# Kernel tuning notes

Hardware: AMD Instinct MI355X
Metric: run time of the kernel (lower is better)

## Reference

```python
import jax, jax.numpy as jnp
import numpy as np

N_NODES = 20000
N_RELS = 64
RP = 8
EMB = 64
N_CLASSES = 16
NT = 250000      # unique (subject, object) pairs
N_TRIPLES = 500000


def setup_inputs() -> dict:
    rng = np.random.default_rng(0)
    # sample candidate (s, o) pairs, dedupe (mirrors torch.unique(pairs, dim=0)),
    # keep exactly NT unique pairs
    cand = rng.integers(0, N_NODES, size=(NT + 60000, 2))
    pairs = np.unique(cand, axis=0)
    assert pairs.shape[0] >= NT
    pairs = pairs[:NT]
    # each triple maps to a unique-pair row and a relation column;
    # relation_matrix is the coalesced sparse_coo (nt, num_rels) densified
    row = rng.integers(0, NT, size=N_TRIPLES)
    rel = rng.integers(0, N_RELS, size=N_TRIPLES)
    relation_matrix = np.zeros((NT, N_RELS), dtype=np.float32)
    np.add.at(relation_matrix, (row, rel), 1.0)
    # hindices / vindices exactly as in __init__ (note the literal o*r / s*r):
    s, o = pairs[:, 0].astype(np.int64), pairs[:, 1].astype(np.int64)
    rm = np.arange(RP, dtype=np.int64)[:, None]
    hrow = np.tile(s, RP)                      # (RP*NT,) row in [0, N)
    hcol = (o[None, :] * rm).reshape(-1)       # (RP*NT,) col in [0, N*RP)
    vrow = (s[None, :] * rm).reshape(-1)       # (RP*NT,) row in [0, N*RP)
    vcol = np.tile(o, RP)                      # (RP*NT,) col in [0, N)

    key = jax.random.key(0)
    ks = jax.random.split(key, 6)

    def xavier(k, shape, fan_in, fan_out):
        gain = np.float32(np.sqrt(2.0))  # calculate_gain('relu')
        bound = gain * np.float32(np.sqrt(6.0 / (fan_in + fan_out)))
        return jax.random.uniform(k, shape, jnp.float32, -bound, bound)

    lb = np.float32(1.0 / np.sqrt(N_RELS))  # nn.Linear default init bound
    return {
        "relation_matrix": jnp.asarray(relation_matrix),
        "hrow": jnp.asarray(hrow), "hcol": jnp.asarray(hcol),
        "vrow": jnp.asarray(vrow), "vcol": jnp.asarray(vcol),
        "W_l1": jax.random.uniform(ks[0], (N_RELS, RP), jnp.float32, -lb, lb),
        "b_l1": jax.random.uniform(ks[1], (RP,), jnp.float32, -lb, lb),
        "W_l2": jax.random.uniform(ks[2], (N_RELS, RP), jnp.float32, -lb, lb),
        "b_l2": jax.random.uniform(ks[3], (RP,), jnp.float32, -lb, lb),
        "weights1": xavier(ks[4], (RP, N_NODES, EMB), N_NODES * EMB, RP * EMB),
        "weights2": xavier(ks[5], (RP, EMB, N_CLASSES), EMB * N_CLASSES, RP * N_CLASSES),
        "bias1": jnp.zeros((EMB,), jnp.float32),
        "bias2": jnp.zeros((N_CLASSES,), jnp.float32),
    }


def reference(relation_matrix, hrow, hcol, vrow, vcol,
              W_l1, b_l1, W_l2, b_l2, weights1, weights2, bias1, bias2):
    n, rp, e = N_NODES, RP, EMB
    nrp = n * rp
    # ---- hop 1: latent coefficients (to_latent1, ldepth=0 => single Linear)
    l1 = relation_matrix @ W_l1 + b_l1              # (NT, RP)
    l1 = l1.T.reshape(-1)                           # (RP*NT,) r-major, matches h/v index order
    # sum_sparse(hindices, l1, (n, n*rp), row=False): per-edge column-sum normalization
    colsum = jax.ops.segment_sum(l1, hcol, num_segments=nrp)
    l1 = l1 / colsum[hcol]
    # spmm over hindices: out[hrow] += l1 * weights1.view(n*rp, e)[hcol]
    Wflat = weights1.reshape(nrp, e)                # (N*RP, EMB)
    h = jax.ops.segment_sum(l1[:, None] * Wflat[hcol], hrow, num_segments=n)
    h = jax.nn.relu(h + bias1)                      # (N, EMB)
    # ---- hop 2
    l2 = jax.nn.softmax(relation_matrix @ W_l2 + b_l2, axis=1)  # (NT, RP)
    l2 = jax.nn.relu(l2.T.reshape(-1))              # (RP*NT,)
    # sum_sparse(vindices, l2, (n*rp, n), row=True): per-edge row-sum normalization
    rowsum = jax.ops.segment_sum(l2, vrow, num_segments=nrp)
    l2 = l2 / jnp.maximum(rowsum[vrow], 1e-6)
    # spmm over vindices: out[vrow] += l2 * h[vcol]
    h2 = jax.ops.segment_sum(l2[:, None] * h[vcol], vrow, num_segments=nrp)
    h2 = h2.reshape(rp, n, e)                       # (RP, N, EMB)
    logits = jnp.einsum('rhc,rnh->nc', weights2, h2) + bias2  # (N, C)
    return logits
```

## Files before the change

### kernel.cpp

```cpp
#include <hip/hip_runtime.h>
#include <hip/hip_fp16.h>

#define NT      250000
#define NN      20000
#define RP      8
#define EMB     64
#define NCLS    16
#define NRELS   64
#define COLB    547
#define REDB    64
#define KMAX    140000

__global__ __launch_bounds__(256) void k_gemv(
    const float* __restrict__ rm,
    const float* __restrict__ W1, const float* __restrict__ b1,
    const float* __restrict__ W2, const float* __restrict__ b2,
    float* __restrict__ l1, float* __restrict__ l2)
{
    __shared__ float tile[256 * 20];
    int t = threadIdx.x;
    int base = blockIdx.x * 256;
    float a1[8], a2[8];
#pragma unroll
    for (int r = 0; r < 8; ++r) { a1[r] = b1[r]; a2[r] = b2[r]; }

#pragma unroll 1
    for (int kc = 0; kc < 4; ++kc) {
        __syncthreads();
#pragma unroll
        for (int q = 0; q < 4; ++q) {
            int i = q * 256 + t;
            int pl = i >> 2, j4 = i & 3;
            int p = base + pl;
            float4 v = make_float4(0.f, 0.f, 0.f, 0.f);
            if (p < NT) v = reinterpret_cast<const float4*>(rm)[(size_t)p * 16 + kc * 4 + j4];
            *reinterpret_cast<float4*>(&tile[pl * 20 + j4 * 4]) = v;
        }
        __syncthreads();
        float xr[16];
#pragma unroll
        for (int j4 = 0; j4 < 4; ++j4) {
            float4 v = *reinterpret_cast<const float4*>(&tile[t * 20 + j4 * 4]);
            xr[j4 * 4 + 0] = v.x; xr[j4 * 4 + 1] = v.y;
            xr[j4 * 4 + 2] = v.z; xr[j4 * 4 + 3] = v.w;
        }
#pragma unroll
        for (int kk = 0; kk < 16; ++kk) {
            float x = xr[kk];
            int k = kc * 16 + kk;
#pragma unroll
            for (int r = 0; r < 8; ++r) {
                a1[r] = fmaf(x, W1[k * 8 + r], a1[r]);
                a2[r] = fmaf(x, W2[k * 8 + r], a2[r]);
            }
        }
    }
    int p = base + t;
    if (p >= NT) return;
    float mx = a2[0];
#pragma unroll
    for (int r = 1; r < 8; ++r) mx = fmaxf(mx, a2[r]);
    float sm = 0.f;
#pragma unroll
    for (int r = 0; r < 8; ++r) { a2[r] = __expf(a2[r] - mx); sm += a2[r]; }
    float inv = 1.0f / sm;
#pragma unroll
    for (int r = 0; r < 8; ++r) a2[r] *= inv;
    float4* o1 = reinterpret_cast<float4*>(l1 + (size_t)p * 8);
    float4* o2 = reinterpret_cast<float4*>(l2 + (size_t)p * 8);
    o1[0] = make_float4(a1[0], a1[1], a1[2], a1[3]);
    o1[1] = make_float4(a1[4], a1[5], a1[6], a1[7]);
    o2[0] = make_float4(a2[0], a2[1], a2[2], a2[3]);
    o2[1] = make_float4(a2[4], a2[5], a2[6], a2[7]);
}

__global__ __launch_bounds__(256) void k_rowptr(
    const int* __restrict__ hrow, int* __restrict__ rowptr)
{
    int i = blockIdx.x * blockDim.x + threadIdx.x;
    if (i > NN) return;
    int lo = 0, hi = NT;
    while (lo < hi) { int mid = (lo + hi) >> 1; if (hrow[mid] < i) lo = mid + 1; else hi = mid; }
    rowptr[i] = lo;
}

__global__ __launch_bounds__(256) void k_hist(
    const int* __restrict__ vcol, int* __restrict__ cnt)
{
    int p = blockIdx.x * blockDim.x + threadIdx.x;
    if (p < NT) atomicAdd(&cnt[vcol[p]], 1);
}

__global__ __launch_bounds__(1024) void k_scan(
    const int* __restrict__ cnt, int* __restrict__ cstart, int* __restrict__ cnt2)
{
    __shared__ int part[1024];
    int t = threadIdx.x;
    int base = t * 20;
    int local[20];
    int s = 0;
#pragma unroll
    for (int i = 0; i < 20; ++i) {
        int idx = base + i;
        int c = (idx < NN) ? cnt[idx] : 0;
        local[i] = s;
        s += c;
    }
    part[t] = s;
    __syncthreads();
    for (int off = 1; off < 1024; off <<= 1) {
        int v = (t >= off) ? part[t - off] : 0;
        __syncthreads();
        part[t] += v;
        __syncthreads();
    }
    int ebase = t ? part[t - 1] : 0;
#pragma unroll
    for (int i = 0; i < 20; ++i) {
        int idx = base + i;
        if (idx < NN) { cstart[idx] = ebase + local[i]; cnt2[idx] = ebase + local[i]; }
    }
    if (t == 1023) cstart[NN] = part[1023];
}

__global__ __launch_bounds__(256) void k_pos(
    const int* __restrict__ vcol, int* __restrict__ cnt2, int* __restrict__ cscidx)
{
    int p = blockIdx.x * blockDim.x + threadIdx.x;
    if (p >= NT) return;
    int o = vcol[p];
    int slot = atomicAdd(&cnt2[o], 1);
    cscidx[slot] = p;
}

__global__ __launch_bounds__(256) void k_colsum(
    const float* __restrict__ l1, const int* __restrict__ cstart,
    const int* __restrict__ cscidx, float* __restrict__ colsum)
{
    int bid = blockIdx.x;
    if (bid < COLB) {
        int tid = bid * 256 + threadIdx.x;
        if (tid < NN * 7) {
            int o = tid / 7;
            int r = tid - o * 7 + 1;
            int qb = cstart[o], qe = cstart[o + 1];
            float s = 0.f;
            for (int q = qb; q < qe; ++q)
                s += l1[(size_t)cscidx[q] * 8 + r];
            atomicAdd(&colsum[o * r], s);
        }
    } else {
        int b2 = bid - COLB;
        float s = 0.f;
        for (int i = b2 * 256 + threadIdx.x; i < NT; i += REDB * 256) s += l1[(size_t)i * 8];
        __shared__ float red[256];
        red[threadIdx.x] = s;
        __syncthreads();
        for (int off = 128; off > 0; off >>= 1) {
            if (threadIdx.x < off) red[threadIdx.x] += red[threadIdx.x + off];
            __syncthreads();
        }
        if (threadIdx.x == 0) atomicAdd(&colsum[0], red[0]);
    }
}

__global__ __launch_bounds__(256) void k_inv(float* __restrict__ cs)
{
    int i = blockIdx.x * blockDim.x + threadIdx.x;
    if (i < RP * NN) cs[i] = 1.0f / cs[i];
}

__global__ __launch_bounds__(256) void k_contrib(
    const float* __restrict__ l1, const float* __restrict__ ics,
    const int* __restrict__ cstart, const int* __restrict__ cscidx,
    const float* __restrict__ w1, __half* __restrict__ contrib)
{
    int o = (int)((blockIdx.x * blockDim.x + threadIdx.x) >> 6);
    int lane = threadIdx.x & 63;
    if (o >= NN) return;
    int qb = cstart[o], qe = cstart[o + 1];
    if (qb == qe) return;
    float y[8];
    y[0] = w1[lane] * ics[0];
#pragma unroll
    for (int r = 1; r < 8; ++r) {
        int seg = o * r;
        y[r] = w1[(size_t)seg * EMB + lane] * ics[seg];
    }
    for (int q = qb; q < qe; ++q) {
        int p = cscidx[q];
        const float4* lp4 = reinterpret_cast<const float4*>(l1 + (size_t)p * 8);
        float4 A = lp4[0], B = lp4[1];
        float v = A.x * y[0];
        v = fmaf(A.y, y[1], v); v = fmaf(A.z, y[2], v); v = fmaf(A.w, y[3], v);
        v = fmaf(B.x, y[4], v); v = fmaf(B.y, y[5], v);
        v = fmaf(B.z, y[6], v); v = fmaf(B.w, y[7], v);
        contrib[(size_t)p * EMB + lane] = __float2half(v);
    }
}

__global__ __launch_bounds__(256) void k_h(
    const __half* __restrict__ contrib, const float* __restrict__ l2,
    const int* __restrict__ rowptr, const float* __restrict__ bias1,
    __half* __restrict__ h, float* __restrict__ rowsum, float* __restrict__ rs0part)
{
    int s = (int)((blockIdx.x * blockDim.x + threadIdx.x) >> 6);
    int lane = threadIdx.x & 63;
    if (s >= NN) return;
    int pb = rowptr[s], pe = rowptr[s + 1];
    float acc = 0.f;
    for (int p = pb; p < pe; ++p)
        acc += __half2float(contrib[(size_t)p * EMB + lane]);
    h[(size_t)s * EMB + lane] = __float2half(fmaxf(acc + bias1[lane], 0.f));

    float psum = 0.f;
    for (int p0 = pb + (lane >> 3); p0 < pe; p0 += 8)
        psum += l2[(size_t)p0 * 8 + (lane & 7)];
    psum += __shfl_xor(psum, 8, 64);
    psum += __shfl_xor(psum, 16, 64);
    psum += __shfl_xor(psum, 32, 64);
    if (s == 0) {
        float tt = psum;
        tt += __shfl_xor(tt, 1, 64);
        tt += __shfl_xor(tt, 2, 64);
        tt += __shfl_xor(tt, 4, 64);
        if (lane == 0) rs0part[0] = tt;
    } else {
        if (lane == 0) rs0part[s] = psum;
        else if (lane < 8) atomicAdd(&rowsum[s * lane], psum);
    }
}

__global__ __launch_bounds__(256) void k_redrs(
    const float* __restrict__ rs0part, float* __restrict__ rowsum)
{
    __shared__ float red[256];
    float sv = 0.f;
    for (int i = threadIdx.x; i < NN; i += 256) sv += rs0part[i];
    red[threadIdx.x] = sv;
    __syncthreads();
    for (int off = 128; off > 0; off >>= 1) {
        if (threadIdx.x < off) red[threadIdx.x] += red[threadIdx.x + off];
        __syncthreads();
    }
    if (threadIdx.x == 0) rowsum[0] = 1.0f / fmaxf(red[0], 1e-6f);
}

__global__ __launch_bounds__(256) void k_inv2(float* __restrict__ rs)
{
    int i = blockIdx.x * blockDim.x + threadIdx.x;
    if (i >= 1 && i < KMAX) rs[i] = 1.0f / fmaxf(rs[i], 1e-6f);
}

__global__ __launch_bounds__(256) void k_outinit(
    float* __restrict__ out, const float* __restrict__ b2)
{
    int i = blockIdx.x * blockDim.x + threadIdx.x;
    if (i < NN * NCLS) out[i] = b2[i & (NCLS - 1)];
}

__global__ __launch_bounds__(256) void k_l2out(
    const float* __restrict__ l2, const int* __restrict__ rowptr,
    const int* __restrict__ vcol, const __half* __restrict__ h,
    const float* __restrict__ irs, const float* __restrict__ w2,
    float* __restrict__ out, float* __restrict__ Abuf0)
{
    int s = (int)((blockIdx.x * blockDim.x + threadIdx.x) >> 6);
    int lane = threadIdx.x & 63;
    if (s >= NN) return;
    int pb = rowptr[s], pe = rowptr[s + 1];
    float acc[8];
#pragma unroll
    for (int r = 0; r < 8; ++r) acc[r] = 0.f;
    int p = pb;
    for (; p + 1 < pe; p += 2) {
        int o0 = vcol[p], o1 = vcol[p + 1];
        float hv0 = __half2float(h[(size_t)o0 * EMB + lane]);
        float hv1 = __half2float(h[(size_t)o1 * EMB + lane]);
        const float4* q4 = reinterpret_cast<const float4*>(l2 + (size_t)p * 8);
        float4 A = q4[0], B = q4[1], C = q4[2], D = q4[3];
        acc[0] = fmaf(A.x, hv0, fmaf(C.x, hv1, acc[0]));
        acc[1] = fmaf(A.y, hv0, fmaf(C.y, hv1, acc[1]));
        acc[2] = fmaf(A.z, hv0, fmaf(C.z, hv1, acc[2]));
        acc[3] = fmaf(A.w, hv0, fmaf(C.w, hv1, acc[3]));
        acc[4] = fmaf(B.x, hv0, fmaf(D.x, hv1, acc[4]));
        acc[5] = fmaf(B.y, hv0, fmaf(D.y, hv1, acc[5]));
        acc[6] = fmaf(B.z, hv0, fmaf(D.z, hv1, acc[6]));
        acc[7] = fmaf(B.w, hv0, fmaf(D.w, hv1, acc[7]));
    }
    if (p < pe) {
        int o0 = vcol[p];
        float hv0 = __half2float(h[(size_t)o0 * EMB + lane]);
        const float4* q4 = reinterpret_cast<const float4*>(l2 + (size_t)p * 8);
        float4 A = q4[0], B = q4[1];
        acc[0] = fmaf(A.x, hv0, acc[0]); acc[1] = fmaf(A.y, hv0, acc[1]);
        acc[2] = fmaf(A.z, hv0, acc[2]); acc[3] = fmaf(A.w, hv0, acc[3]);
        acc[4] = fmaf(B.x, hv0, acc[4]); acc[5] = fmaf(B.y, hv0, acc[5]);
        acc[6] = fmaf(B.z, hv0, acc[6]); acc[7] = fmaf(B.w, hv0, acc[7]);
    }
    if (s == 0) {
        float a = acc[0] + acc[1] + acc[2] + acc[3] +
                  acc[4] + acc[5] + acc[6] + acc[7];
        Abuf0[lane] = a;
        return;
    }
    Abuf0[(size_t)s * EMB + lane] = acc[0];
    if (pb == pe) return;
    int hq = lane >> 4, c = lane & 15;
#pragma unroll
    for (int rr = 1; rr < 8; ++rr) {
        int k = s * rr;
        int rp = k / NN;
        int n  = k - rp * NN;
        float sc = irs[k];
        float v = 0.f;
#pragma unroll
        for (int hh = 0; hh < 16; ++hh) {
            float av = __shfl(acc[rr], hq * 16 + hh, 64);
            v = fmaf(av, w2[((rp * EMB) + (hq * 16 + hh)) * NCLS + c], v);
        }
        v += __shfl_xor(v, 16, 64);
        v += __shfl_xor(v, 32, 64);
        if (lane < 16) atomicAdd(&out[(size_t)n * NCLS + lane], v * sc);
    }
}

__global__ __launch_bounds__(256) void k_redA(
    const float* __restrict__ Abuf0, float* __restrict__ h0row)
{
    __shared__ float red[256];
    int lane = threadIdx.x & 63, w = threadIdx.x >> 6;
    float sum = 0.f;
    for (int ss = blockIdx.x + 64 * w; ss < NN; ss += 256)
        sum += Abuf0[(size_t)ss * EMB + lane];
    red[threadIdx.x] = sum;
    __syncthreads();
    if (threadIdx.x < 64) {
        float v = red[threadIdx.x] + red[threadIdx.x + 64] +
                  red[threadIdx.x + 128] + red[threadIdx.x + 192];
        atomicAdd(&h0row[threadIdx.x], v);
    }
}

__global__ __launch_bounds__(64) void k_out0(
    const float* __restrict__ h0row, const float* __restrict__ irs,
    const float* __restrict__ w2, float* __restrict__ out)
{
    int hq = threadIdx.x >> 4, c = threadIdx.x & 15;
    float v = 0.f;
#pragma unroll
    for (int hh = 0; hh < 16; ++hh) {
        int hd = hq * 16 + hh;
        v = fmaf(h0row[hd], w2[hd * NCLS + c], v);
    }
    v += __shfl_xor(v, 16, 64);
    v += __shfl_xor(v, 32, 64);
    if (threadIdx.x < 16) atomicAdd(&out[c], v * irs[0]);
}

extern "C" void kernel_launch(void* const* d_in, const int* in_sizes, int n_in,
                              void* d_out, int out_size, void* d_ws, size_t ws_size,
                              hipStream_t stream)
{
    const float* rm    = (const float*)d_in[0];
    const int*   hrow  = (const int*)d_in[1];
    const int*   vcol  = (const int*)d_in[4];
    const float* W1    = (const float*)d_in[5];
    const float* b1    = (const float*)d_in[6];
    const float* W2    = (const float*)d_in[7];
    const float* b2    = (const float*)d_in[8];
    const float* w1    = (const float*)d_in[9];
    const float* w2    = (const float*)d_in[10];
    const float* bias1 = (const float*)d_in[11];
    const float* bias2 = (const float*)d_in[12];
    float* out = (float*)d_out;

    float* ws = (float*)d_ws;
    float*  l1      = ws;
    float*  l2      = ws + 2000000;
    int*    rowptr  = (int*)(ws + 4000000);
    float*  h0row   = ws + 4030000;
    float*  colsum  = ws + 4100000;
    float*  rowsum  = ws + 4260000;
    __half* h       = (__half*)(ws + 4400000);
    int*    cnt     = (int*)(ws + 5040000);
    int*    cstart  = cnt + 20000;
    int*    cnt2    = cstart + 20001;
    int*    cscidx  = cnt2 + 20000;
    __half* contrib = (__half*)(ws + 5600000);
    float*  Abuf0   = ws;
    float*  rs0part = ws + 1280000;

    hipMemsetAsync(colsum, 0, (size_t)160000 * sizeof(float), stream);
    hipMemsetAsync(rowsum, 0, (size_t)KMAX * sizeof(float), stream);
    hipMemsetAsync(h0row, 0, (size_t)64 * sizeof(float), stream);
    hipMemsetAsync(cnt, 0, (size_t)20000 * sizeof(int), stream);

    k_rowptr <<<(NN + 256) / 256, 256, 0, stream>>>(hrow, rowptr);
    k_hist   <<<(NT + 255) / 256, 256, 0, stream>>>(vcol, cnt);
    k_scan   <<<1, 1024, 0, stream>>>(cnt, cstart, cnt2);
    k_pos    <<<(NT + 255) / 256, 256, 0, stream>>>(vcol, cnt2, cscidx);
    k_gemv   <<<(NT + 255) / 256, 256, 0, stream>>>(rm, W1, b1, W2, b2, l1, l2);
    k_colsum <<<COLB + REDB, 256, 0, stream>>>(l1, cstart, cscidx, colsum);
    k_inv    <<<(RP * NN + 255) / 256, 256, 0, stream>>>(colsum);
    k_contrib<<<(NN * 64) / 256, 256, 0, stream>>>(l1, colsum, cstart, cscidx, w1, contrib);
    k_h      <<<(NN * 64) / 256, 256, 0, stream>>>(contrib, l2, rowptr, bias1, h, rowsum, rs0part);
    k_redrs  <<<1, 256, 0, stream>>>(rs0part, rowsum);
    k_inv2   <<<(KMAX + 255) / 256, 256, 0, stream>>>(rowsum);
    k_outinit<<<(NN * NCLS + 255) / 256, 256, 0, stream>>>(out, bias2);
    k_l2out  <<<(NN * 64) / 256, 256, 0, stream>>>(l2, rowptr, vcol, h, rowsum, w2, out, Abuf0);
    k_redA   <<<64, 256, 0, stream>>>(Abuf0, h0row);
    k_out0   <<<1, 64, 0, stream>>>(h0row, rowsum, w2, out);
}
```

Before: 261.8 us.

## Scatter l1 into CSC order and rewrite colsum as wave-per-column reduction

k_gemv now writes l1 rows directly in column-sorted (CSC) order using a position array recorded by k_pos. This lets colsum and contrib read l1 contiguously instead of gathering through cscidx. colsum becomes one wavefront per column with shuffle reductions, plus a separate reduction kernel for column 0. Smaller changes merge the inv2 and outinit kernels, unroll the k_l2out loop by 4, and hoist the row-scale loads. The cost is an extra index array, a scattered write in gemv, and one more tiny kernel launch.

```diff
diff --git a/kernel.cpp b/kernel.cpp
--- a/kernel.cpp
+++ b/kernel.cpp
@@ -7,15 +7,14 @@
 #define EMB     64
 #define NCLS    16
 #define NRELS   64
-#define COLB    547
-#define REDB    64
 #define KMAX    140000
 
 __global__ __launch_bounds__(256) void k_gemv(
     const float* __restrict__ rm,
     const float* __restrict__ W1, const float* __restrict__ b1,
     const float* __restrict__ W2, const float* __restrict__ b2,
-    float* __restrict__ l1, float* __restrict__ l2)
+    const int* __restrict__ cscpos,
+    float* __restrict__ l1csc, float* __restrict__ l2)
 {
     __shared__ float tile[256 * 20];
     int t = threadIdx.x;
@@ -66,7 +65,8 @@
     float inv = 1.0f / sm;
 #pragma unroll
     for (int r = 0; r < 8; ++r) a2[r] *= inv;
-    float4* o1 = reinterpret_cast<float4*>(l1 + (size_t)p * 8);
+    int q = cscpos[p];
+    float4* o1 = reinterpret_cast<float4*>(l1csc + (size_t)q * 8);
     float4* o2 = reinterpret_cast<float4*>(l2 + (size_t)p * 8);
     o1[0] = make_float4(a1[0], a1[1], a1[2], a1[3]);
     o1[1] = make_float4(a1[4], a1[5], a1[6], a1[7]);
@@ -124,44 +124,60 @@
 }
 
 __global__ __launch_bounds__(256) void k_pos(
-    const int* __restrict__ vcol, int* __restrict__ cnt2, int* __restrict__ cscidx)
+    const int* __restrict__ vcol, int* __restrict__ cnt2,
+    int* __restrict__ cscidx, int* __restrict__ cscpos)
 {
     int p = blockIdx.x * blockDim.x + threadIdx.x;
     if (p >= NT) return;
     int o = vcol[p];
     int slot = atomicAdd(&cnt2[o], 1);
     cscidx[slot] = p;
+    cscpos[p] = slot;
 }
 
 __global__ __launch_bounds__(256) void k_colsum(
-    const float* __restrict__ l1, const int* __restrict__ cstart,
-    const int* __restrict__ cscidx, float* __restrict__ colsum)
-{
-    int bid = blockIdx.x;
-    if (bid < COLB) {
-        int tid = bid * 256 + threadIdx.x;
-        if (tid < NN * 7) {
-            int o = tid / 7;
-            int r = tid - o * 7 + 1;
-            int qb = cstart[o], qe = cstart[o + 1];
-            float s = 0.f;
-            for (int q = qb; q < qe; ++q)
-                s += l1[(size_t)cscidx[q] * 8 + r];
-            atomicAdd(&colsum[o * r], s);
-        }
+    const float* __restrict__ l1csc, const int* __restrict__ cstart,
+    float* __restrict__ colsum, float* __restrict__ cs0part)
+{
+    int o = (int)((blockIdx.x * blockDim.x + threadIdx.x) >> 6);
+    int lane = threadIdx.x & 63;
+    if (o >= NN) return;
+    int qb = cstart[o], qe = cstart[o + 1];
+    if (qb == qe) { if (lane == 0) cs0part[o] = 0.f; return; }
+    int j = lane >> 3, r = lane & 7;
+    float sum = 0.f;
+    for (int q0 = qb; q0 < qe; q0 += 8) {
+        int q = q0 + j;
+        if (q < qe) sum += l1csc[(size_t)q * 8 + r];
+    }
+    sum += __shfl_xor(sum, 8, 64);
+    sum += __shfl_xor(sum, 16, 64);
+    sum += __shfl_xor(sum, 32, 64);
+    if (o == 0) {
+        float tt = sum;
+        tt += __shfl_xor(tt, 1, 64);
+        tt += __shfl_xor(tt, 2, 64);
+        tt += __shfl_xor(tt, 4, 64);
+        if (lane == 0) cs0part[0] = tt;
     } else {
-        int b2 = bid - COLB;
-        float s = 0.f;
-        for (int i = b2 * 256 + threadIdx.x; i < NT; i += REDB * 256) s += l1[(size_t)i * 8];
-        __shared__ float red[256];
-        red[threadIdx.x] = s;
-        __syncthreads();
-        for (int off = 128; off > 0; off >>= 1) {
-            if (threadIdx.x < off) red[threadIdx.x] += red[threadIdx.x + off];
-            __syncthreads();
-        }
-        if (threadIdx.x == 0) atomicAdd(&colsum[0], red[0]);
-    }
+        if (lane == 0) cs0part[o] = sum;
+        else if (lane < 8) atomicAdd(&colsum[o * lane], sum);
+    }
+}
+
+__global__ __launch_bounds__(256) void k_redcs(
+    const float* __restrict__ cs0part, float* __restrict__ colsum)
+{
+    __shared__ float red[256];
+    float sv = 0.f;
+    for (int i = threadIdx.x; i < NN; i += 256) sv += cs0part[i];
+    red[threadIdx.x] = sv;
+    __syncthreads();
+    for (int off = 128; off > 0; off >>= 1) {
+        if (threadIdx.x < off) red[threadIdx.x] += red[threadIdx.x + off];
+        __syncthreads();
+    }
+    if (threadIdx.x == 0) colsum[0] = red[0];
 }
 
 __global__ __launch_bounds__(256) void k_inv(float* __restrict__ cs)
@@ -171,7 +187,7 @@
 }
 
 __global__ __launch_bounds__(256) void k_contrib(
-    const float* __restrict__ l1, const float* __restrict__ ics,
+    const float* __restrict__ l1csc, const float* __restrict__ ics,
     const int* __restrict__ cstart, const int* __restrict__ cscidx,
     const float* __restrict__ w1, __half* __restrict__ contrib)
 {
@@ -188,13 +204,13 @@
         y[r] = w1[(size_t)seg * EMB + lane] * ics[seg];
     }
     for (int q = qb; q < qe; ++q) {
-        int p = cscidx[q];
-        const float4* lp4 = reinterpret_cast<const float4*>(l1 + (size_t)p * 8);
+        const float4* lp4 = reinterpret_cast<const float4*>(l1csc + (size_t)q * 8);
         float4 A = lp4[0], B = lp4[1];
         float v = A.x * y[0];
         v = fmaf(A.y, y[1], v); v = fmaf(A.z, y[2], v); v = fmaf(A.w, y[3], v);
         v = fmaf(B.x, y[4], v); v = fmaf(B.y, y[5], v);
         v = fmaf(B.z, y[6], v); v = fmaf(B.w, y[7], v);
+        int p = cscidx[q];
         contrib[(size_t)p * EMB + lane] = __float2half(v);
     }
 }
@@ -246,16 +262,11 @@
     if (threadIdx.x == 0) rowsum[0] = 1.0f / fmaxf(red[0], 1e-6f);
 }
 
-__global__ __launch_bounds__(256) void k_inv2(float* __restrict__ rs)
+__global__ __launch_bounds__(256) void k_misc(
+    float* __restrict__ rs, float* __restrict__ out, const float* __restrict__ b2)
 {
     int i = blockIdx.x * blockDim.x + threadIdx.x;
     if (i >= 1 && i < KMAX) rs[i] = 1.0f / fmaxf(rs[i], 1e-6f);
-}
-
-__global__ __launch_bounds__(256) void k_outinit(
-    float* __restrict__ out, const float* __restrict__ b2)
-{
-    int i = blockIdx.x * blockDim.x + threadIdx.x;
     if (i < NN * NCLS) out[i] = b2[i & (NCLS - 1)];
 }
 
@@ -269,26 +280,32 @@
     int lane = threadIdx.x & 63;
     if (s >= NN) return;
     int pb = rowptr[s], pe = rowptr[s + 1];
+    float sc[8];
+#pragma unroll
+    for (int rr = 1; rr < 8; ++rr) sc[rr] = (s > 0) ? irs[s * rr] : 0.f;
     float acc[8];
 #pragma unroll
     for (int r = 0; r < 8; ++r) acc[r] = 0.f;
     int p = pb;
-    for (; p + 1 < pe; p += 2) {
-        int o0 = vcol[p], o1 = vcol[p + 1];
+    for (; p + 3 < pe; p += 4) {
+        int o0 = vcol[p], o1 = vcol[p + 1], o2 = vcol[p + 2], o3 = vcol[p + 3];
         float hv0 = __half2float(h[(size_t)o0 * EMB + lane]);
         float hv1 = __half2float(h[(size_t)o1 * EMB + lane]);
+        float hv2 = __half2float(h[(size_t)o2 * EMB + lane]);
+        float hv3 = __half2float(h[(size_t)o3 * EMB + lane]);
         const float4* q4 = reinterpret_cast<const float4*>(l2 + (size_t)p * 8);
         float4 A = q4[0], B = q4[1], C = q4[2], D = q4[3];
-        acc[0] = fmaf(A.x, hv0, fmaf(C.x, hv1, acc[0]));
-        acc[1] = fmaf(A.y, hv0, fmaf(C.y, hv1, acc[1]));
-        acc[2] = fmaf(A.z, hv0, fmaf(C.z, hv1, acc[2]));
-        acc[3] = fmaf(A.w, hv0, fmaf(C.w, hv1, acc[3]));
-        acc[4] = fmaf(B.x, hv0, fmaf(D.x, hv1, acc[4]));
-        acc[5] = fmaf(B.y, hv0, fmaf(D.y, hv1, acc[5]));
-        acc[6] = fmaf(B.z, hv0, fmaf(D.z, hv1, acc[6]));
-        acc[7] = fmaf(B.w, hv0, fmaf(D.w, hv1, acc[7]));
-    }
-    if (p < pe) {
+        float4 E = q4[4], F = q4[5], G = q4[6], H = q4[7];
+        acc[0] = fmaf(A.x, hv0, fmaf(C.x, hv1, fmaf(E.x, hv2, fmaf(G.x, hv3, acc[0]))));
+        acc[1] = fmaf(A.y, hv0, fmaf(C.y, hv1, fmaf(E.y, hv2, fmaf(G.y, hv3, acc[1]))));
+        acc[2] = fmaf(A.z, hv0, fmaf(C.z, hv1, fmaf(E.z, hv2, fmaf(G.z, hv3, acc[2]))));
+        acc[3] = fmaf(A.w, hv0, fmaf(C.w, hv1, fmaf(E.w, hv2, fmaf(G.w, hv3, acc[3]))));
+        acc[4] = fmaf(B.x, hv0, fmaf(D.x, hv1, fmaf(F.x, hv2, fmaf(H.x, hv3, acc[4]))));
+        acc[5] = fmaf(B.y, hv0, fmaf(D.y, hv1, fmaf(F.y, hv2, fmaf(H.y, hv3, acc[5]))));
+        acc[6] = fmaf(B.z, hv0, fmaf(D.z, hv1, fmaf(F.z, hv2, fmaf(H.z, hv3, acc[6]))));
+        acc[7] = fmaf(B.w, hv0, fmaf(D.w, hv1, fmaf(F.w, hv2, fmaf(H.w, hv3, acc[7]))));
+    }
+    for (; p < pe; ++p) {
         int o0 = vcol[p];
         float hv0 = __half2float(h[(size_t)o0 * EMB + lane]);
         const float4* q4 = reinterpret_cast<const float4*>(l2 + (size_t)p * 8);
@@ -312,7 +329,6 @@
         int k = s * rr;
         int rp = k / NN;
         int n  = k - rp * NN;
-        float sc = irs[k];
         float v = 0.f;
 #pragma unroll
         for (int hh = 0; hh < 16; ++hh) {
@@ -321,7 +337,7 @@
         }
         v += __shfl_xor(v, 16, 64);
         v += __shfl_xor(v, 32, 64);
-        if (lane < 16) atomicAdd(&out[(size_t)n * NCLS + lane], v * sc);
+        if (lane < 16) atomicAdd(&out[(size_t)n * NCLS + lane], v * sc[rr]);
     }
 }
 
@@ -376,10 +392,11 @@
     float* out = (float*)d_out;
 
     float* ws = (float*)d_ws;
-    float*  l1      = ws;
+    float*  l1csc   = ws;
     float*  l2      = ws + 2000000;
     int*    rowptr  = (int*)(ws + 4000000);
     float*  h0row   = ws + 4030000;
+    float*  cs0part = ws + 4032000;
     float*  colsum  = ws + 4100000;
     float*  rowsum  = ws + 4260000;
     __half* h       = (__half*)(ws + 4400000);
@@ -387,7 +404,8 @@
     int*    cstart  = cnt + 20000;
     int*    cnt2    = cstart + 20001;
     int*    cscidx  = cnt2 + 20000;
-    __half* contrib = (__half*)(ws + 5600000);
+    int*    cscpos  = (int*)(ws + 5360000);
+    __half* contrib = (__half*)(ws + 5700000);
     float*  Abuf0   = ws;
     float*  rs0part = ws + 1280000;
 
@@ -399,15 +417,15 @@
     k_rowptr <<<(NN + 256) / 256, 256, 0, stream>>>(hrow, rowptr);
     k_hist   <<<(NT + 255) / 256, 256, 0, stream>>>(vcol, cnt);
     k_scan   <<<1, 1024, 0, stream>>>(cnt, cstart, cnt2);
-    k_pos    <<<(NT + 255) / 256, 256, 0, stream>>>(vcol, cnt2, cscidx);
-    k_gemv   <<<(NT + 255) / 256, 256, 0, stream>>>(rm, W1, b1, W2, b2, l1, l2);
-    k_colsum <<<COLB + REDB, 256, 0, stream>>>(l1, cstart, cscidx, colsum);
+    k_pos    <<<(NT + 255) / 256, 256, 0, stream>>>(vcol, cnt2, cscidx, cscpos);
+    k_gemv   <<<(NT + 255) / 256, 256, 0, stream>>>(rm, W1, b1, W2, b2, cscpos, l1csc, l2);
+    k_colsum <<<(NN * 64) / 256, 256, 0, stream>>>(l1csc, cstart, colsum, cs0part);
+    k_redcs  <<<1, 256, 0, stream>>>(cs0part, colsum);
     k_inv    <<<(RP * NN + 255) / 256, 256, 0, stream>>>(colsum);
-    k_contrib<<<(NN * 64) / 256, 256, 0, stream>>>(l1, colsum, cstart, cscidx, w1, contrib);
+    k_contrib<<<(NN * 64) / 256, 256, 0, stream>>>(l1csc, colsum, cstart, cscidx, w1, contrib);
     k_h      <<<(NN * 64) / 256, 256, 0, stream>>>(contrib, l2, rowptr, bias1, h, rowsum, rs0part);
     k_redrs  <<<1, 256, 0, stream>>>(rs0part, rowsum);
-    k_inv2   <<<(KMAX + 255) / 256, 256, 0, stream>>>(rowsum);
-    k_outinit<<<(NN * NCLS + 255) / 256, 256, 0, stream>>>(out, bias2);
+    k_misc   <<<(NN * NCLS + 255) / 256, 256, 0, stream>>>(rowsum, out, bias2);
     k_l2out  <<<(NN * 64) / 256, 256, 0, stream>>>(l2, rowptr, vcol, h, rowsum, w2, out, Abuf0);
     k_redA   <<<64, 256, 0, stream>>>(Abuf0, h0row);
     k_out0   <<<1, 64, 0, stream>>>(h0row, rowsum, w2, out);
```

Measured after the change: 269.4 us. 2.9% more time.

## Split each hop-2 row across two wavefronts and merge the init kernels

Applied to the files above, without the earlier changes.

The hop-2 SpMM kernel now gives each source row to two wavefronts. Each wavefront takes half the edges with a 4-way unrolled loop, and the partial accumulators are combined through shared memory. The seven class-projection atomics are also split between the two wavefronts, and the scale factors are prefetched before the edge loop. The inverse-rowsum and output-init kernels are fused into one launch. This adds more parallelism and memory-level overlap on long rows and removes one launch, at the cost of a block barrier, shared-memory traffic and idle wavefronts on short rows.

```diff
diff --git a/kernel.cpp b/kernel.cpp
--- a/kernel.cpp
+++ b/kernel.cpp
@@ -246,16 +246,11 @@
     if (threadIdx.x == 0) rowsum[0] = 1.0f / fmaxf(red[0], 1e-6f);
 }
 
-__global__ __launch_bounds__(256) void k_inv2(float* __restrict__ rs)
+__global__ __launch_bounds__(256) void k_misc(
+    float* __restrict__ rs, float* __restrict__ out, const float* __restrict__ b2)
 {
     int i = blockIdx.x * blockDim.x + threadIdx.x;
     if (i >= 1 && i < KMAX) rs[i] = 1.0f / fmaxf(rs[i], 1e-6f);
-}
-
-__global__ __launch_bounds__(256) void k_outinit(
-    float* __restrict__ out, const float* __restrict__ b2)
-{
-    int i = blockIdx.x * blockDim.x + threadIdx.x;
     if (i < NN * NCLS) out[i] = b2[i & (NCLS - 1)];
 }
 
@@ -265,30 +260,41 @@
     const float* __restrict__ irs, const float* __restrict__ w2,
     float* __restrict__ out, float* __restrict__ Abuf0)
 {
-    int s = (int)((blockIdx.x * blockDim.x + threadIdx.x) >> 6);
+    __shared__ float lacc[4][8 * 64];
+    int w = threadIdx.x >> 6;
     int lane = threadIdx.x & 63;
-    if (s >= NN) return;
+    int g = w >> 1, sub = w & 1;
+    int s = blockIdx.x * 2 + g;
     int pb = rowptr[s], pe = rowptr[s + 1];
+    float sc[8];
+#pragma unroll
+    for (int rr = 1; rr < 8; ++rr) sc[rr] = (s > 0) ? irs[s * rr] : 0.f;
     float acc[8];
 #pragma unroll
     for (int r = 0; r < 8; ++r) acc[r] = 0.f;
-    int p = pb;
-    for (; p + 1 < pe; p += 2) {
-        int o0 = vcol[p], o1 = vcol[p + 1];
+    int half = (pe - pb + 1) >> 1;
+    int mb = pb + sub * half;
+    int me = sub ? pe : pb + half;
+    int p = mb;
+    for (; p + 3 < me; p += 4) {
+        int o0 = vcol[p], o1 = vcol[p + 1], o2 = vcol[p + 2], o3 = vcol[p + 3];
         float hv0 = __half2float(h[(size_t)o0 * EMB + lane]);
         float hv1 = __half2float(h[(size_t)o1 * EMB + lane]);
+        float hv2 = __half2float(h[(size_t)o2 * EMB + lane]);
+        float hv3 = __half2float(h[(size_t)o3 * EMB + lane]);
         const float4* q4 = reinterpret_cast<const float4*>(l2 + (size_t)p * 8);
         float4 A = q4[0], B = q4[1], C = q4[2], D = q4[3];
-        acc[0] = fmaf(A.x, hv0, fmaf(C.x, hv1, acc[0]));
-        acc[1] = fmaf(A.y, hv0, fmaf(C.y, hv1, acc[1]));
-        acc[2] = fmaf(A.z, hv0, fmaf(C.z, hv1, acc[2]));
-        acc[3] = fmaf(A.w, hv0, fmaf(C.w, hv1, acc[3]));
-        acc[4] = fmaf(B.x, hv0, fmaf(D.x, hv1, acc[4]));
-        acc[5] = fmaf(B.y, hv0, fmaf(D.y, hv1, acc[5]));
-        acc[6] = fmaf(B.z, hv0, fmaf(D.z, hv1, acc[6]));
-        acc[7] = fmaf(B.w, hv0, fmaf(D.w, hv1, acc[7]));
-    }
-    if (p < pe) {
+        float4 E = q4[4], F = q4[5], G = q4[6], H = q4[7];
+        acc[0] = fmaf(A.x, hv0, fmaf(C.x, hv1, fmaf(E.x, hv2, fmaf(G.x, hv3, acc[0]))));
+        acc[1] = fmaf(A.y, hv0, fmaf(C.y, hv1, fmaf(E.y, hv2, fmaf(G.y, hv3, acc[1]))));
+        acc[2] = fmaf(A.z, hv0, fmaf(C.z, hv1, fmaf(E.z, hv2, fmaf(G.z, hv3, acc[2]))));
+        acc[3] = fmaf(A.w, hv0, fmaf(C.w, hv1, fmaf(E.w, hv2, fmaf(G.w, hv3, acc[3]))));
+        acc[4] = fmaf(B.x, hv0, fmaf(D.x, hv1, fmaf(F.x, hv2, fmaf(H.x, hv3, acc[4]))));
+        acc[5] = fmaf(B.y, hv0, fmaf(D.y, hv1, fmaf(F.y, hv2, fmaf(H.y, hv3, acc[5]))));
+        acc[6] = fmaf(B.z, hv0, fmaf(D.z, hv1, fmaf(F.z, hv2, fmaf(H.z, hv3, acc[6]))));
+        acc[7] = fmaf(B.w, hv0, fmaf(D.w, hv1, fmaf(F.w, hv2, fmaf(H.w, hv3, acc[7]))));
+    }
+    for (; p < me; ++p) {
         int o0 = vcol[p];
         float hv0 = __half2float(h[(size_t)o0 * EMB + lane]);
         const float4* q4 = reinterpret_cast<const float4*>(l2 + (size_t)p * 8);
@@ -298,30 +304,38 @@
         acc[4] = fmaf(B.x, hv0, acc[4]); acc[5] = fmaf(B.y, hv0, acc[5]);
         acc[6] = fmaf(B.z, hv0, acc[6]); acc[7] = fmaf(B.w, hv0, acc[7]);
     }
+#pragma unroll
+    for (int r = 0; r < 8; ++r) lacc[w][r * 64 + lane] = acc[r];
+    __syncthreads();
+    float ca[8];
+#pragma unroll
+    for (int r = 0; r < 8; ++r)
+        ca[r] = lacc[2 * g][r * 64 + lane] + lacc[2 * g + 1][r * 64 + lane];
     if (s == 0) {
-        float a = acc[0] + acc[1] + acc[2] + acc[3] +
-                  acc[4] + acc[5] + acc[6] + acc[7];
-        Abuf0[lane] = a;
+        if (sub == 0) {
+            float a = ca[0] + ca[1] + ca[2] + ca[3] + ca[4] + ca[5] + ca[6] + ca[7];
+            Abuf0[lane] = a;
+        }
         return;
     }
-    Abuf0[(size_t)s * EMB + lane] = acc[0];
+    if (sub == 0) Abuf0[(size_t)s * EMB + lane] = ca[0];
     if (pb == pe) return;
     int hq = lane >> 4, c = lane & 15;
-#pragma unroll
-    for (int rr = 1; rr < 8; ++rr) {
+    int rlo = sub ? 4 : 1, rhi = sub ? 8 : 4;
+    for (int rr = rlo; rr < rhi; ++rr) {
         int k = s * rr;
         int rp = k / NN;
         int n  = k - rp * NN;
-        float sc = irs[k];
+        float a = ca[rr];
         float v = 0.f;
 #pragma unroll
         for (int hh = 0; hh < 16; ++hh) {
-            float av = __shfl(acc[rr], hq * 16 + hh, 64);
+            float av = __shfl(a, hq * 16 + hh, 64);
             v = fmaf(av, w2[((rp * EMB) + (hq * 16 + hh)) * NCLS + c], v);
         }
         v += __shfl_xor(v, 16, 64);
         v += __shfl_xor(v, 32, 64);
-        if (lane < 16) atomicAdd(&out[(size_t)n * NCLS + lane], v * sc);
+        if (lane < 16) atomicAdd(&out[(size_t)n * NCLS + lane], v * sc[rr]);
     }
 }
 
@@ -343,7 +357,7 @@
 }
 
 __global__ __launch_bounds__(64) void k_out0(
-    const float* __restrict__ h0row, const float* __restrict__ irs,
+    const float* __restrict__ h0row, const float* __restrict__ irs0,
     const float* __restrict__ w2, float* __restrict__ out)
 {
     int hq = threadIdx.x >> 4, c = threadIdx.x & 15;
@@ -355,7 +369,7 @@
     }
     v += __shfl_xor(v, 16, 64);
     v += __shfl_xor(v, 32, 64);
-    if (threadIdx.x < 16) atomicAdd(&out[c], v * irs[0]);
+    if (threadIdx.x < 16) atomicAdd(&out[c], v * irs0[0]);
 }
 
 extern "C" void kernel_launch(void* const* d_in, const int* in_sizes, int n_in,
@@ -406,9 +420,8 @@
     k_contrib<<<(NN * 64) / 256, 256, 0, stream>>>(l1, colsum, cstart, cscidx, w1, contrib);
     k_h      <<<(NN * 64) / 256, 256, 0, stream>>>(contrib, l2, rowptr, bias1, h, rowsum, rs0part);
     k_redrs  <<<1, 256, 0, stream>>>(rs0part, rowsum);
-    k_inv2   <<<(KMAX + 255) / 256, 256, 0, stream>>>(rowsum);
-    k_outinit<<<(NN * NCLS + 255) / 256, 256, 0, stream>>>(out, bias2);
-    k_l2out  <<<(NN * 64) / 256, 256, 0, stream>>>(l2, rowptr, vcol, h, rowsum, w2, out, Abuf0);
+    k_misc   <<<(NN * NCLS + 255) / 256, 256, 0, stream>>>(rowsum, out, bias2);
+    k_l2out  <<<NN / 2, 256, 0, stream>>>(l2, rowptr, vcol, h, rowsum, w2, out, Abuf0);
     k_redA   <<<64, 256, 0, stream>>>(Abuf0, h0row);
     k_out0   <<<1, 64, 0, stream>>>(h0row, rowsum, w2, out);
 }
```

After: 264.9 us. No clear change (+1.2%).
